# Kernel tuning notes

Hardware: AMD Instinct MI355X
Metric: run time of the kernel (lower is better)

## Reference

```python
import jax, jax.numpy as jnp
import numpy as np

N = 50000   # nodes
E = 800000  # edges
F = 128     # feat_dim
LN_EPS = 1e-5


def setup_inputs() -> dict:
    key = jax.random.key(0)
    ks = jax.random.split(key, 16)

    def lin(k, fan_in, shape):
        # roughly kaiming-uniform-like scale; exact init is irrelevant for correctness
        return jax.random.normal(k, shape, jnp.float32) * (1.0 / np.sqrt(fan_in))

    inp = {
        "x": jax.random.normal(ks[0], (N, F), jnp.float32),
        "pos": jax.random.normal(ks[1], (N, 3), jnp.float32),
        "edge_index": jax.random.randint(ks[2], (2, E), 0, N, jnp.int64),
        # edge_mlp: Linear(2F+1 -> F), SiLU, Linear(F -> F)
        "ew1": lin(ks[3], 2 * F + 1, (2 * F + 1, F)),
        "eb1": jnp.zeros((F,), jnp.float32),
        "ew2": lin(ks[4], F, (F, F)),
        "eb2": jnp.zeros((F,), jnp.float32),
        # node_mlp: Linear(F -> F), SiLU, Linear(F -> F)
        "nw1": lin(ks[5], F, (F, F)),
        "nb1": jnp.zeros((F,), jnp.float32),
        "nw2": lin(ks[6], F, (F, F)),
        "nb2": jnp.zeros((F,), jnp.float32),
        # coord_mlp: Linear(F -> 1), Tanh
        "cw": lin(ks[7], F, (F, 1)),
        "cb": jnp.zeros((1,), jnp.float32),
        # LayerNorm(F)
        "gamma": jnp.ones((F,), jnp.float32),
        "beta": jnp.zeros((F,), jnp.float32),
    }
    return inp


def reference(x, pos, edge_index, ew1, eb1, ew2, eb2, nw1, nb1, nw2, nb2, cw, cb, gamma, beta):
    row, col = edge_index[0], edge_index[1]

    diff = pos[row] - pos[col]                              # [E, 3]
    dist2 = jnp.sum(diff * diff, axis=1, keepdims=True)     # [E, 1]
    edge_feat = jnp.concatenate([x[row], x[col], dist2], axis=1)  # [E, 2F+1]

    # edge MLP (dropout p=0 -> identity in eval)
    msg = jax.nn.silu(edge_feat @ ew1 + eb1) @ ew2 + eb2    # [E, F]

    # scatter-add messages to source nodes
    agg = jax.ops.segment_sum(msg, row, num_segments=N)     # [N, F]

    # node MLP + residual + LayerNorm
    upd = jax.nn.silu(agg @ nw1 + nb1) @ nw2 + nb2          # [N, F]
    pre = x + upd
    mean = jnp.mean(pre, axis=-1, keepdims=True)
    var = jnp.mean(jnp.square(pre - mean), axis=-1, keepdims=True)
    x_out = gamma * (pre - mean) * jax.lax.rsqrt(var + LN_EPS) + beta

    # coordinate update
    scale = jnp.tanh(msg @ cw + cb)                         # [E, 1]
    delta = jax.ops.segment_sum(scale * diff, row, num_segments=N)  # [N, 3]
    pos_out = pos + delta
    return (x_out, pos_out)
```

## Files before the change

### kernel.cpp

```cpp
#include <hip/hip_runtime.h>
#include <math.h>

#define NN 50000
#define EE 800000
#define FF 128

constexpr float LN_EPS = 1e-5f;
constexpr int NC = (NN + 255) / 256;

typedef float  f32x4  __attribute__((ext_vector_type(4)));
typedef short  s16x8  __attribute__((ext_vector_type(8)));
typedef unsigned short u16x4 __attribute__((ext_vector_type(4)));

__device__ __forceinline__ float silu_f(float v) {
    return v / (1.f + __expf(-v));
}

__device__ __forceinline__ unsigned short f2bf(float f) {
    union { float f; unsigned u; } cv; cv.f = f;
    unsigned u = cv.u;
    u += 0x7fffu + ((u >> 16) & 1u);
    return (unsigned short)(u >> 16);
}

__device__ __forceinline__ float bf2f(unsigned short u) {
    union { unsigned u; float f; } cv; cv.u = ((unsigned)u) << 16;
    return cv.f;
}

constexpr int CVT_BLKS = (NN * FF / 8) / 256;
constexpr int TRW_BLKS = (32768 + 3 * 16384) / 256;

__global__ __launch_bounds__(256) void prep_kernel(
    const float* __restrict__ x, unsigned short* __restrict__ xb,
    const float* __restrict__ ew1, const float* __restrict__ ew2,
    const float* __restrict__ nw1, const float* __restrict__ nw2,
    unsigned short* __restrict__ ew1T, unsigned short* __restrict__ ew2T,
    unsigned short* __restrict__ nw1T, unsigned short* __restrict__ nw2T)
{
    if (blockIdx.x < CVT_BLKS) {
        int i = (blockIdx.x * 256 + threadIdx.x) * 8;
        float4 a = *(const float4*)&x[i];
        float4 b = *(const float4*)&x[i + 4];
        s16x8 o;
        o[0] = (short)f2bf(a.x); o[1] = (short)f2bf(a.y);
        o[2] = (short)f2bf(a.z); o[3] = (short)f2bf(a.w);
        o[4] = (short)f2bf(b.x); o[5] = (short)f2bf(b.y);
        o[6] = (short)f2bf(b.z); o[7] = (short)f2bf(b.w);
        *(s16x8*)&xb[i] = o;
    } else {
        int o = (blockIdx.x - CVT_BLKS) * 256 + threadIdx.x;
        if (o < 32768) {
            int n = o >> 8, k = o & 255;
            ew1T[o] = f2bf(ew1[k * FF + n]);
        } else if (o < 49152) {
            int o2 = o - 32768; int n = o2 >> 7, k = o2 & 127;
            ew2T[o2] = f2bf(ew2[k * FF + n]);
        } else if (o < 65536) {
            int o2 = o - 49152; int n = o2 >> 7, k = o2 & 127;
            nw1T[o2] = f2bf(nw1[k * FF + n]);
        } else {
            int o2 = o - 65536; int n = o2 >> 7, k = o2 & 127;
            nw2T[o2] = f2bf(nw2[k * FF + n]);
        }
    }
}

__global__ __launch_bounds__(256) void hist_kernel(
    const int* __restrict__ ei, int* __restrict__ cnt)
{
    int e = blockIdx.x * 256 + threadIdx.x;
    if (e < EE) atomicAdd(&cnt[ei[e]], 1);
}

__global__ __launch_bounds__(256) void chunk_sum_kernel(
    const int* __restrict__ cnt, int* __restrict__ chunkSum)
{
    __shared__ int s[256];
    int t = threadIdx.x;
    int idx = blockIdx.x * 256 + t;
    s[t] = (idx < NN) ? cnt[idx] : 0;
    __syncthreads();
    for (int off = 128; off > 0; off >>= 1) {
        if (t < off) s[t] += s[t + off];
        __syncthreads();
    }
    if (t == 0) chunkSum[blockIdx.x] = s[0];
}

__global__ __launch_bounds__(256) void scan_chunks_kernel(
    const int* __restrict__ chunkSum, int* __restrict__ chunkOff)
{
    __shared__ int s[256];
    int t = threadIdx.x;
    int v = (t < NC) ? chunkSum[t] : 0;
    s[t] = v;
    __syncthreads();
    for (int off = 1; off < 256; off <<= 1) {
        int u = (t >= off) ? s[t - off] : 0;
        __syncthreads();
        s[t] += u;
        __syncthreads();
    }
    if (t < NC) chunkOff[t] = s[t] - v;
}

__global__ __launch_bounds__(256) void scan_kernel(
    const int* __restrict__ cnt, const int* __restrict__ chunkOff,
    int* __restrict__ offs, int* __restrict__ rowStart)
{
    __shared__ int s[256];
    int t = threadIdx.x;
    int idx = blockIdx.x * 256 + t;
    int v = (idx < NN) ? cnt[idx] : 0;
    s[t] = v;
    __syncthreads();
    for (int off = 1; off < 256; off <<= 1) {
        int u = (t >= off) ? s[t - off] : 0;
        __syncthreads();
        s[t] += u;
        __syncthreads();
    }
    if (idx < NN) {
        int st = chunkOff[blockIdx.x] + s[t] - v;
        offs[idx] = st;
        rowStart[idx] = st;
    }
}

__global__ __launch_bounds__(256) void scatter_idx_kernel(
    const int* __restrict__ ei, int* __restrict__ offs,
    int2* __restrict__ sPair)
{
    int e = blockIdx.x * 256 + threadIdx.x;
    if (e < EE) {
        int r = ei[e], c = ei[EE + e];
        int p = atomicAdd(&offs[r], 1);
        sPair[p] = make_int2(r, c);
    }
}

constexpr int EPB    = 64;
constexpr int NTILE  = EE / EPB;
constexpr int GRID_A = 2500;
constexpr int XAS    = 264;
constexpr int H1S    = 136;

__global__ __launch_bounds__(512, 4) void edgeA_kernel(
    const unsigned short* __restrict__ xb, const float* __restrict__ pos,
    const int2* __restrict__ sPair,
    const unsigned short* __restrict__ ew1T, const float* __restrict__ ew1,
    const float* __restrict__ eb1,
    const unsigned short* __restrict__ ew2T, const float* __restrict__ eb2,
    const float* __restrict__ cw,  const float* __restrict__ cb,
    float* __restrict__ agg, float* __restrict__ sSg)
{
    __shared__ float dist2S[EPB];
    __shared__ int   rowS  [EPB];
    __shared__ float sPartT[EPB][8];
    __shared__ __align__(16) unsigned short xa[EPB * XAS];
    __shared__ __align__(16) unsigned short h1[EPB * H1S];
    unsigned short* msgL = xa;

    const int t   = threadIdx.x;
    const int w   = t >> 6;
    const int l   = t & 63;
    const int l15 = l & 15;
    const int q8  = l >> 4;
    const int n   = w * 16 + l15;

    int swz;
    {
        const int qd = GRID_A >> 3, r8 = GRID_A & 7;
        int xcd = blockIdx.x & 7, p8 = blockIdx.x >> 3;
        swz = (xcd < r8 ? xcd * (qd + 1) : r8 * (qd + 1) + (xcd - r8) * qd) + p8;
    }

    s16x8 B1[8], B2[4];
    #pragma unroll
    for (int ko = 0; ko < 8; ++ko)
        B1[ko] = *(const s16x8*)(ew1T + (size_t)n * 256 + ko * 32 + q8 * 8);
    #pragma unroll
    for (int ko = 0; ko < 4; ++ko)
        B2[ko] = *(const s16x8*)(ew2T + (size_t)n * 128 + ko * 32 + q8 * 8);
    const float w256 = ew1[256 * FF + n];
    const float b1   = eb1[n];
    const float b2   = eb2[n];
    const float cwc  = cw[n];
    const float cb0  = cb[0];

    const int q    = t & 31;
    const int eB   = t >> 5;
    const int ksel = (q & 15) * 8;
    const bool useRow = (q < 16);

    int   nidx[4];
    s16x8 ag[4];
    {
        int e0 = swz * EPB;
        #pragma unroll
        for (int i = 0; i < 4; ++i) {
            int2 pr = sPair[e0 + eB + 16 * i];
            nidx[i] = useRow ? pr.x : pr.y;
        }
        #pragma unroll
        for (int i = 0; i < 4; ++i) ag[i] = *(const s16x8*)(xb + (size_t)nidx[i] * FF + ksel);
    }

    for (int tile = swz; tile < NTILE; tile += GRID_A) {
        const int e0 = tile * EPB;

        #pragma unroll
        for (int i = 0; i < 4; ++i)
            *(s16x8*)(xa + (eB + 16 * i) * XAS + q * 8) = ag[i];
        if (t < EPB) {
            int2 pr = sPair[e0 + t];
            int r = pr.x, c = pr.y;
            rowS[t] = r;
            float dx = pos[r*3+0] - pos[c*3+0];
            float dy = pos[r*3+1] - pos[c*3+1];
            float dz = pos[r*3+2] - pos[c*3+2];
            dist2S[t] = dx*dx + dy*dy + dz*dz;
        }
        __syncthreads();

        {
            int tn  = tile + GRID_A;
            int e0n = (tn < NTILE) ? tn * EPB : 0;
            #pragma unroll
            for (int i = 0; i < 4; ++i) {
                int2 pr = sPair[e0n + eB + 16 * i];
                nidx[i] = useRow ? pr.x : pr.y;
            }
            #pragma unroll
            for (int i = 0; i < 4; ++i) ag[i] = *(const s16x8*)(xb + (size_t)nidx[i] * FF + ksel);
        }

        f32x4 acc[4] = {};
        #pragma unroll
        for (int mt = 0; mt < 4; ++mt) {
            const unsigned short* ar = xa + (mt * 16 + l15) * XAS + q8 * 8;
            #pragma unroll
            for (int ko = 0; ko < 8; ++ko) {
                s16x8 a = *(const s16x8*)(ar + ko * 32);
                acc[mt] = __builtin_amdgcn_mfma_f32_16x16x32_bf16(a, B1[ko], acc[mt], 0, 0, 0);
            }
        }

        #pragma unroll
        for (int mt = 0; mt < 4; ++mt) {
            #pragma unroll
            for (int r = 0; r < 4; ++r) {
                int e = mt * 16 + q8 * 4 + r;
                float v = acc[mt][r] + dist2S[e] * w256 + b1;
                h1[e * H1S + n] = f2bf(silu_f(v));
            }
        }
        __syncthreads();

        f32x4 acc2[4] = {};
        #pragma unroll
        for (int mt = 0; mt < 4; ++mt) {
            const unsigned short* hr = h1 + (mt * 16 + l15) * H1S + q8 * 8;
            #pragma unroll
            for (int ko = 0; ko < 4; ++ko) {
                s16x8 a = *(const s16x8*)(hr + ko * 32);
                acc2[mt] = __builtin_amdgcn_mfma_f32_16x16x32_bf16(a, B2[ko], acc2[mt], 0, 0, 0);
            }
        }

        #pragma unroll
        for (int mt = 0; mt < 4; ++mt) {
            #pragma unroll
            for (int r = 0; r < 4; ++r) {
                float m = acc2[mt][r] + b2;
                float p = m * cwc;
                p += __shfl_xor(p, 1);
                p += __shfl_xor(p, 2);
                p += __shfl_xor(p, 4);
                p += __shfl_xor(p, 8);
                int e = mt * 16 + q8 * 4 + r;
                if (l15 == 0) sPartT[e][w] = p;
                msgL[e * H1S + n] = f2bf(m);
            }
        }
        __syncthreads();

        {
            int e  = t >> 3;
            int ww = t & 7;
            float p = sPartT[e][ww];
            p += __shfl_xor(p, 1);
            p += __shfl_xor(p, 2);
            p += __shfl_xor(p, 4);
            if (ww == 0) sSg[e0 + e] = tanhf(p + cb0);
        }

        {
            int c    = t & 127;
            int s    = t >> 7;
            int base = s * 16;
            float a  = 0.f;
            int cur  = rowS[base];
            #pragma unroll
            for (int k = 0; k < 16; ++k) {
                int e = base + k;
                int r = rowS[e];
                if (r != cur) {
                    atomicAdd(&agg[(size_t)cur * FF + c], a);
                    a = 0.f; cur = r;
                }
                a += bf2f(msgL[e * H1S + c]);
            }
            atomicAdd(&agg[(size_t)cur * FF + c], a);
        }
        __syncthreads();
    }
}

constexpr int NPB  = 64;
constexpr int ABS  = 136;
constexpr int NBLK = (NN + NPB - 1) / NPB;

__global__ __launch_bounds__(512) void nodeB_kernel(
    const float* __restrict__ x, const float* __restrict__ pos,
    const float* __restrict__ agg, const float* __restrict__ sSg,
    const int2* __restrict__ sPair, const int* __restrict__ rowStart,
    const unsigned short* __restrict__ nw1T, const float* __restrict__ nb1,
    const unsigned short* __restrict__ nw2T, const float* __restrict__ nb2,
    const float* __restrict__ gamma, const float* __restrict__ beta,
    float* __restrict__ xout, float* __restrict__ posout)
{
    __shared__ __align__(16) unsigned short aB [NPB * ABS];
    __shared__ __align__(16) unsigned short h1B[NPB * ABS];
    __shared__ float sRedS[8][NPB];
    __shared__ float sRedQ[8][NPB];

    const int t   = threadIdx.x;
    const int w   = t >> 6;
    const int l   = t & 63;
    const int l15 = l & 15;
    const int q8  = l >> 4;
    const int n0  = blockIdx.x * NPB;
    const int n   = w * 16 + l15;

    #pragma unroll
    for (int i = 0; i < 4; ++i) {
        int idx = (i * 512 + t) * 4;
        int e = idx >> 7, c = idx & 127;
        u16x4 o;
        if (n0 + e < NN) {
            float4 v = *(const float4*)&agg[(size_t)(n0 + e) * FF + c];
            o[0] = f2bf(v.x); o[1] = f2bf(v.y); o[2] = f2bf(v.z); o[3] = f2bf(v.w);
        } else {
            o[0] = 0; o[1] = 0; o[2] = 0; o[3] = 0;
        }
        *(u16x4*)(aB + e * ABS + c) = o;
    }

    {
        int e  = t >> 3;
        int ch = t & 7;
        int nn = n0 + e;
        bool ok = nn < NN;
        int p0 = ok ? rowStart[nn] : 0;
        int p1 = ok ? ((nn == NN - 1) ? EE : rowStart[nn + 1]) : 0;
        float px = ok ? pos[nn*3+0] : 0.f;
        float py = ok ? pos[nn*3+1] : 0.f;
        float pz = ok ? pos[nn*3+2] : 0.f;
        float sx = 0.f, sy = 0.f, sz = 0.f;
        for (int p = p0 + ch; p < p1; p += 8) {
            int c = sPair[p].y;
            float g = sSg[p];
            sx += g * (px - pos[c*3+0]);
            sy += g * (py - pos[c*3+1]);
            sz += g * (pz - pos[c*3+2]);
        }
        #pragma unroll
        for (int off = 1; off < 8; off <<= 1) {
            sx += __shfl_xor(sx, off);
            sy += __shfl_xor(sy, off);
            sz += __shfl_xor(sz, off);
        }
        if (ch == 0 && ok) {
            posout[nn*3+0] = px + sx;
            posout[nn*3+1] = py + sy;
            posout[nn*3+2] = pz + sz;
        }
    }
    __syncthreads();

    f32x4 acc[4] = {};
    {
        s16x8 bw[4];
        #pragma unroll
        for (int ko = 0; ko < 4; ++ko)
            bw[ko] = *(const s16x8*)(nw1T + (size_t)n * 128 + ko * 32 + q8 * 8);
        #pragma unroll
        for (int mt = 0; mt < 4; ++mt) {
            const unsigned short* ar = aB + (mt * 16 + l15) * ABS + q8 * 8;
            #pragma unroll
            for (int ko = 0; ko < 4; ++ko) {
                s16x8 a = *(const s16x8*)(ar + ko * 32);
                acc[mt] = __builtin_amdgcn_mfma_f32_16x16x32_bf16(a, bw[ko], acc[mt], 0, 0, 0);
            }
        }
    }
    {
        float bb = nb1[n];
        #pragma unroll
        for (int mt = 0; mt < 4; ++mt) {
            #pragma unroll
            for (int r = 0; r < 4; ++r) {
                int e = mt * 16 + q8 * 4 + r;
                h1B[e * ABS + n] = f2bf(silu_f(acc[mt][r] + bb));
            }
        }
    }
    __syncthreads();

    f32x4 acc2[4] = {};
    {
        s16x8 bw[4];
        #pragma unroll
        for (int ko = 0; ko < 4; ++ko)
            bw[ko] = *(const s16x8*)(nw2T + (size_t)n * 128 + ko * 32 + q8 * 8);
        #pragma unroll
        for (int mt = 0; mt < 4; ++mt) {
            const unsigned short* hr = h1B + (mt * 16 + l15) * ABS + q8 * 8;
            #pragma unroll
            for (int ko = 0; ko < 4; ++ko) {
                s16x8 a = *(const s16x8*)(hr + ko * 32);
                acc2[mt] = __builtin_amdgcn_mfma_f32_16x16x32_bf16(a, bw[ko], acc2[mt], 0, 0, 0);
            }
        }
    }

    float pre[4][4];
    {
        float bb = nb2[n];
        #pragma unroll
        for (int mt = 0; mt < 4; ++mt) {
            #pragma unroll
            for (int r = 0; r < 4; ++r) {
                int e  = mt * 16 + q8 * 4 + r;
                int nn = n0 + e;
                float xv = (nn < NN) ? x[(size_t)nn * FF + n] : 0.f;
                pre[mt][r] = xv + acc2[mt][r] + bb;
            }
        }
    }
    #pragma unroll
    for (int mt = 0; mt < 4; ++mt) {
        #pragma unroll
        for (int r = 0; r < 4; ++r) {
            float s = pre[mt][r], sq = pre[mt][r] * pre[mt][r];
            s += __shfl_xor(s, 1);  sq += __shfl_xor(sq, 1);
            s += __shfl_xor(s, 2);  sq += __shfl_xor(sq, 2);
            s += __shfl_xor(s, 4);  sq += __shfl_xor(sq, 4);
            s += __shfl_xor(s, 8);  sq += __shfl_xor(sq, 8);
            if (l15 == 0) {
                int e = mt * 16 + q8 * 4 + r;
                sRedS[w][e] = s;
                sRedQ[w][e] = sq;
            }
        }
    }
    __syncthreads();

    {
        float g = gamma[n], bt = beta[n];
        #pragma unroll
        for (int mt = 0; mt < 4; ++mt) {
            #pragma unroll
            for (int r = 0; r < 4; ++r) {
                int e  = mt * 16 + q8 * 4 + r;
                int nn = n0 + e;
                if (nn < NN) {
                    float S = 0.f, Q = 0.f;
                    #pragma unroll
                    for (int ww = 0; ww < 8; ++ww) { S += sRedS[ww][e]; Q += sRedQ[ww][e]; }
                    float mean = S * (1.f / FF);
                    float var  = Q * (1.f / FF) - mean * mean;
                    xout[(size_t)nn * FF + n] =
                        g * (pre[mt][r] - mean) * rsqrtf(var + LN_EPS) + bt;
                }
            }
        }
    }
}

extern "C" void kernel_launch(void* const* d_in, const int* in_sizes, int n_in,
                              void* d_out, int out_size, void* d_ws, size_t ws_size,
                              hipStream_t stream) {
    const float* x    = (const float*)d_in[0];
    const float* pos  = (const float*)d_in[1];
    const int*   ei   = (const int*)  d_in[2];
    const float* ew1  = (const float*)d_in[3];
    const float* eb1  = (const float*)d_in[4];
    const float* ew2  = (const float*)d_in[5];
    const float* eb2  = (const float*)d_in[6];
    const float* nw1  = (const float*)d_in[7];
    const float* nb1  = (const float*)d_in[8];
    const float* nw2  = (const float*)d_in[9];
    const float* nb2  = (const float*)d_in[10];
    const float* cw   = (const float*)d_in[11];
    const float* cb   = (const float*)d_in[12];
    const float* gam  = (const float*)d_in[13];
    const float* bet  = (const float*)d_in[14];

    float* out    = (float*)d_out;
    float* xout   = out;
    float* posout = out + (size_t)NN * FF;

    auto align256 = [](size_t v) { return (v + 255) & ~(size_t)255; };
    char* ws = (char*)d_ws;

    size_t CNT_B   = align256((size_t)NN * 4);
    size_t OFFS_B  = align256((size_t)NN * 4);
    size_t RST_B   = align256((size_t)NN * 4);
    size_t CHNK_B  = align256((size_t)NC * 4 * 2);
    size_t SPAIR_B = align256((size_t)EE * 8);
    size_t XB_B    = align256((size_t)NN * FF * 2);
    size_t EW1T_B  = align256((size_t)128 * 256 * 2);
    size_t WT_B    = align256((size_t)128 * 128 * 2);
    size_t AGG_B   = align256((size_t)NN * FF * 4);

    size_t o = 0;
    int* cnt       = (int*)(ws + o);  o += CNT_B;
    int* offs      = (int*)(ws + o);  o += OFFS_B;
    int* rowStart  = (int*)(ws + o);  o += RST_B;
    int* chunkSum  = (int*)(ws + o);
    int* chunkOff  = chunkSum + NC;   o += CHNK_B;
    int2* sPair    = (int2*)(ws + o); o += SPAIR_B;
    unsigned short* xb   = (unsigned short*)(ws + o);  o += XB_B;
    unsigned short* ew1T = (unsigned short*)(ws + o);  o += EW1T_B;
    unsigned short* ew2T = (unsigned short*)(ws + o);  o += WT_B;
    unsigned short* nw1T = (unsigned short*)(ws + o);  o += WT_B;
    unsigned short* nw2T = (unsigned short*)(ws + o);  o += WT_B;
    float*          agg  = (float*)(ws + o);           o += AGG_B;
    float*          sSg  = (float*)(ws + o);

    hipMemsetAsync(cnt, 0, CNT_B, stream);
    hipMemsetAsync(agg, 0, (size_t)NN * FF * 4, stream);

    prep_kernel<<<CVT_BLKS + TRW_BLKS, 256, 0, stream>>>(
        x, xb, ew1, ew2, nw1, nw2, ew1T, ew2T, nw1T, nw2T);

    hist_kernel<<<(EE + 255) / 256, 256, 0, stream>>>(ei, cnt);
    chunk_sum_kernel<<<NC, 256, 0, stream>>>(cnt, chunkSum);
    scan_chunks_kernel<<<1, 256, 0, stream>>>(chunkSum, chunkOff);
    scan_kernel<<<NC, 256, 0, stream>>>(cnt, chunkOff, offs, rowStart);
    scatter_idx_kernel<<<(EE + 255) / 256, 256, 0, stream>>>(ei, offs, sPair);

    edgeA_kernel<<<GRID_A, 512, 0, stream>>>(
        xb, pos, sPair, ew1T, ew1, eb1, ew2T, eb2, cw, cb, agg, sSg);

    nodeB_kernel<<<NBLK, 512, 0, stream>>>(
        x, pos, agg, sSg, sPair, rowStart,
        nw1T, nb1, nw2T, nb2, gam, bet, xout, posout);
}
```

Baseline: 498.9 us.

## Transpose msg into separate LDS buffer and drop trailing tile barrier

Messages are now written transposed into a dedicated LDS buffer (feature-major) with 4-wide vector stores, so the segmented scatter reads 16 edges per channel with two 16-byte loads instead of 16 scalar strided reads. Because msg no longer aliases xa, and rowS is double-buffered by tile parity, the final __syncthreads at the end of each tile iteration is removed, letting the next tile's xa staging overlap the previous scatter. LDS use rises by about 18KB per block, which may lower occupancy at 4 blocks per CU.

```diff
diff --git a/kernel.cpp b/kernel.cpp
--- a/kernel.cpp
+++ b/kernel.cpp
@@ -145,6 +145,7 @@
 constexpr int GRID_A = 2500;
 constexpr int XAS    = 264;
 constexpr int H1S    = 136;
+constexpr int MTS    = 72;
 
 __global__ __launch_bounds__(512, 4) void edgeA_kernel(
     const unsigned short* __restrict__ xb, const float* __restrict__ pos,
@@ -156,11 +157,11 @@
     float* __restrict__ agg, float* __restrict__ sSg)
 {
     __shared__ float dist2S[EPB];
-    __shared__ int   rowS  [EPB];
+    __shared__ int   rowS[2][EPB];
     __shared__ float sPartT[EPB][8];
-    __shared__ __align__(16) unsigned short xa[EPB * XAS];
-    __shared__ __align__(16) unsigned short h1[EPB * H1S];
-    unsigned short* msgL = xa;
+    __shared__ __align__(16) unsigned short xa  [EPB * XAS];
+    __shared__ __align__(16) unsigned short h1  [EPB * H1S];
+    __shared__ __align__(16) unsigned short msgT[FF * MTS];
 
     const int t   = threadIdx.x;
     const int w   = t >> 6;
@@ -207,6 +208,7 @@
         for (int i = 0; i < 4; ++i) ag[i] = *(const s16x8*)(xb + (size_t)nidx[i] * FF + ksel);
     }
 
+    int bsel = 0;
     for (int tile = swz; tile < NTILE; tile += GRID_A) {
         const int e0 = tile * EPB;
 
@@ -216,7 +218,7 @@
         if (t < EPB) {
             int2 pr = sPair[e0 + t];
             int r = pr.x, c = pr.y;
-            rowS[t] = r;
+            rowS[bsel][t] = r;
             float dx = pos[r*3+0] - pos[c*3+0];
             float dy = pos[r*3+1] - pos[c*3+1];
             float dz = pos[r*3+2] - pos[c*3+2];
@@ -271,18 +273,19 @@
 
         #pragma unroll
         for (int mt = 0; mt < 4; ++mt) {
+            u16x4 o;
             #pragma unroll
             for (int r = 0; r < 4; ++r) {
                 float m = acc2[mt][r] + b2;
+                o[r] = f2bf(m);
                 float p = m * cwc;
                 p += __shfl_xor(p, 1);
                 p += __shfl_xor(p, 2);
                 p += __shfl_xor(p, 4);
                 p += __shfl_xor(p, 8);
-                int e = mt * 16 + q8 * 4 + r;
-                if (l15 == 0) sPartT[e][w] = p;
-                msgL[e * H1S + n] = f2bf(m);
-            }
+                if (l15 == 0) sPartT[mt * 16 + q8 * 4 + r][w] = p;
+            }
+            *(u16x4*)(msgT + n * MTS + mt * 16 + q8 * 4) = o;
         }
         __syncthreads();
 
@@ -300,21 +303,25 @@
             int c    = t & 127;
             int s    = t >> 7;
             int base = s * 16;
+            const unsigned short* mr = msgT + c * MTS + base;
+            s16x8 v0 = *(const s16x8*)(mr);
+            s16x8 v1 = *(const s16x8*)(mr + 8);
             float a  = 0.f;
-            int cur  = rowS[base];
+            int cur  = rowS[bsel][base];
             #pragma unroll
             for (int k = 0; k < 16; ++k) {
-                int e = base + k;
-                int r = rowS[e];
+                int r = rowS[bsel][base + k];
                 if (r != cur) {
                     atomicAdd(&agg[(size_t)cur * FF + c], a);
                     a = 0.f; cur = r;
                 }
-                a += bf2f(msgL[e * H1S + c]);
+                unsigned short mv = (k < 8) ? (unsigned short)v0[k]
+                                            : (unsigned short)v1[k - 8];
+                a += bf2f(mv);
             }
             atomicAdd(&agg[(size_t)cur * FF + c], a);
         }
-        __syncthreads();
+        bsel ^= 1;
     }
 }
 
```

New measurement: 494.9 us. No clear change (-0.8%).
